# Kernel optimization log

Measured on AMD Instinct MI355X. Metric: run time of the kernel, lower is better.

Reference implementation:

```python
import math
import jax, jax.numpy as jnp
import numpy as np

CHUNK = 64  # chunk_size


def sinusoidal_pe(L, H):
    # PositionalEncoding2: standard sinusoidal table added to input (eval mode, no dropout)
    pos = jnp.arange(L, dtype=jnp.float32)[:, None]
    div = jnp.exp(jnp.arange(0, H, 2, dtype=jnp.float32) * (-math.log(10000.0) / H))
    pe = jnp.zeros((L, H), dtype=jnp.float32)
    pe = pe.at[:, 0::2].set(jnp.sin(pos * div))
    pe = pe.at[:, 1::2].set(jnp.cos(pos * div))
    return pe


def setup_inputs() -> dict:
    key = jax.random.key(0)
    ks = jax.random.split(key, 8)
    B, T, D, H, Dv = 8, 4096, 512, 512, 512
    s = 0.02
    return {
        "data": jax.random.normal(ks[0], (B, T, D), dtype=jnp.float32),
        "v0": jax.random.normal(ks[1], (B, Dv), dtype=jnp.float32),
        "v1": jax.random.normal(ks[2], (B, Dv), dtype=jnp.float32),
        "W_embed": jax.random.normal(ks[3], (D, H), dtype=jnp.float32) * s,
        "b_embed": jnp.zeros((H,), dtype=jnp.float32),
        "Wx": jax.random.normal(ks[4], (H, 2), dtype=jnp.float32) * s,
        "Wv": jax.random.normal(ks[5], (Dv, 2), dtype=jnp.float32) * s,
        "b_f": jnp.zeros((2,), dtype=jnp.float32),
    }


def reference(data, v0, v1, W_embed, b_embed, Wx, Wv, b_f):
    B, T, D = data.shape
    H = W_embed.shape[1]
    n_chunks = T // CHUNK  # chunks per batch row

    # add_pos: Linear embed + positional encoding, scaled by sqrt(chunk_size)
    h = data @ W_embed + b_embed                       # [B, T, H]
    h = (h + sinusoidal_pe(T, H)[None]) * math.sqrt(CHUNK)

    x = h.reshape(B * n_chunks, CHUNK, H)              # chunked view

    key = jax.random.key(42)
    F = None
    for i, v in enumerate((v0, v1)):
        v_rep = jnp.repeat(v, n_chunks, axis=0)        # [B*n_chunks, Dv]
        # filter model: per-token 2-way logits conditioned on chunk value vector
        logits = x @ Wx + (v_rep @ Wv)[:, None, :] + b_f  # [B*n_chunks, CHUNK, 2]
        # StochasticMultinomialTensor.sample(): gumbel-max one-hot, straight-through
        g = jax.random.gumbel(jax.random.fold_in(key, i), logits.shape, dtype=logits.dtype)
        hard = jax.nn.one_hot(jnp.argmax(logits + g, axis=-1), 2, dtype=logits.dtype)
        soft = jax.nn.softmax(logits, axis=-1)
        samp = soft + jax.lax.stop_gradient(hard - soft)
        f = samp[:, :, 0].reshape(B, T)                # de_chunk -> [B, T]
        F = f if F is None else F * f

    mask = F > 0.5                                     # [B, T]
    vals = h * F[..., None]                            # data[F>0.5] * F scaling

    # ragged compaction: stable-sort selected tokens to the front of each row
    order = jnp.argsort((~mask).astype(jnp.int32), axis=1)   # stable
    packed = jnp.take_along_axis(vals, order[:, :, None], axis=1)  # [B, T, H]
    lens = mask.sum(-1)                                # per-row selected count
    keep = jnp.arange(T)[None, :] < lens[:, None]
    # pad_sequence equivalent, padded to T (superset of max(lens)); zeros beyond lens
    return packed * keep[..., None]
```

## Files before the change

### kernel.cpp

```cpp
#include <hip/hip_runtime.h>
#include <stdint.h>


#define NB 8
#define NT 4096
#define ND 512
#define NH 512
#define NTOK (NB * NT)

typedef __attribute__((ext_vector_type(8))) short short8;
typedef __attribute__((ext_vector_type(4))) float f32x4;

#define WS_WEX   0
#define WS_PEX   8192
#define WS_VWV   73728
#define WS_LENS  76048
#define WS_WT    76096
#define WS_MASK  731456
#define WS_ABF16 1310720

__device__ inline void threefry2x32(uint32_t k0, uint32_t k1, uint32_t x0, uint32_t x1,
                                    uint32_t& y0, uint32_t& y1) {
  uint32_t ks2 = k0 ^ k1 ^ 0x1BD11BDAu;
  x0 += k0; x1 += k1;
#define TFR(r) { x0 += x1; x1 = (x1 << (r)) | (x1 >> (32 - (r))); x1 ^= x0; }
  TFR(13) TFR(15) TFR(26) TFR(6)   x0 += k1;  x1 += ks2 + 1u;
  TFR(17) TFR(29) TFR(16) TFR(24)  x0 += ks2; x1 += k0 + 2u;
  TFR(13) TFR(15) TFR(26) TFR(6)   x0 += k0;  x1 += k1 + 3u;
  TFR(17) TFR(29) TFR(16) TFR(24)  x0 += k1;  x1 += ks2 + 4u;
  TFR(13) TFR(15) TFR(26) TFR(6)   x0 += ks2; x1 += k0 + 5u;
#undef TFR
  y0 = x0; y1 = x1;
}

__device__ inline uint32_t rb_bits(uint32_t k0, uint32_t k1, uint32_t idx) {
  uint32_t y0, y1;
  threefry2x32(k0, k1, 0u, idx, y0, y1);
  return y0 ^ y1;
}

__device__ inline double gumbel_from_bits(uint32_t bits) {
  uint32_t m = bits >> 9;
  float u = m ? (float)m * 1.1920928955078125e-07f : 1.17549435082228751e-38f;
  double lu = log((double)u);
  return -log(-lu);
}

__device__ inline uint16_t f2bf(float f) {
  union { float f; uint32_t u; } v; v.f = f;
  uint32_t u = v.u;
  return (uint16_t)((u + 0x7FFFu + ((u >> 16) & 1u)) >> 16);
}

__device__ inline double wredd(double v) {
#pragma unroll
  for (int o = 32; o > 0; o >>= 1) v += __shfl_xor(v, o, 64);
  return v;
}

__device__ inline void fsincos(double x, double& sv, double& cv) {
  const double invpio2 = 6.36619772367581382433e-01;
  const double pio2_1  = 1.57079632673412561417e+00;
  const double pio2_1t = 6.07710050650619224932e-11;
  double fn = floor(x * invpio2 + 0.5);
  int n = (int)fn;
  double r = x - fn * pio2_1;
  r = r - fn * pio2_1t;
  double z = r * r;
  const double S1 = -1.66666666666666324348e-01, S2 = 8.33333333332248946124e-03,
               S3 = -1.98412698298579493134e-04, S4 = 2.75573137070700676789e-06,
               S5 = -2.50507602534068634195e-08, S6 = 1.58969099521155010221e-10;
  const double C1 = 4.16666666666666019037e-02, C2 = -1.38888888888741095749e-03,
               C3 = 2.48015872894767294178e-05, C4 = -2.75573143513906633035e-07,
               C5 = 2.08757232129817482790e-09, C6 = -1.13596475577881948265e-11;
  double ss = r + r * z * (S1 + z * (S2 + z * (S3 + z * (S4 + z * (S5 + z * S6)))));
  double cc = 1.0 + z * (-0.5 + z * (C1 + z * (C2 + z * (C3 + z * (C4 + z * (C5 + z * C6))))));
  int q = n & 3;
  sv = (q == 0) ? ss : (q == 1) ? cc : (q == 2) ? -ss : -cc;
  cv = (q == 0) ? cc : (q == 1) ? -ss : (q == 2) ? -cc : ss;
}

__device__ inline void gld_lds16(const void* g, void* l) {
  __builtin_amdgcn_global_load_lds(
      (const __attribute__((address_space(1))) void*)g,
      (__attribute__((address_space(3))) void*)l, 16, 0, 0);
}

__global__ __launch_bounds__(64) void k_prep(
    const float* __restrict__ v0, const float* __restrict__ v1,
    const float* __restrict__ W, const float* __restrict__ be,
    const float* __restrict__ Wx, const float* __restrict__ Wv,
    char* __restrict__ ws) {
  double* Wex = (double*)(ws + WS_WEX);
  double* pex = (double*)(ws + WS_PEX);
  double* vWv = (double*)(ws + WS_VWV);
  uint16_t* Wt = (uint16_t*)(ws + WS_WT);
  __shared__ double divs[256];
  int blk = blockIdx.x;
  int lane = threadIdx.x;

  if (blk < 512) {
    int d = blk;
    double a0 = 0.0, a1 = 0.0;
    for (int it = 0; it < 8; ++it) {
      int h = it * 64 + lane;
      double w = (double)W[d * 512 + h];
      a0 += w * (double)Wx[2 * h];
      a1 += w * (double)Wx[2 * h + 1];
    }
    a0 = wredd(a0); a1 = wredd(a1);
    if (lane == 0) { Wex[2 * d] = a0; Wex[2 * d + 1] = a1; }
  } else if (blk < 4608) {
    const double c2 = -2.0 * 9.210340371976184 / 512.0;
    for (int it = 0; it < 4; ++it) {
      int f = it * 64 + lane;
      divs[f] = exp((double)f * c2);
    }
    __syncthreads();
    int t = blk - 512;
    double td = (double)t;
    double a0 = 0.0, a1 = 0.0;
    for (int it = 0; it < 8; ++it) {
      int h = it * 64 + lane;
      double dv = divs[h >> 1];
      double sv, cv;
      fsincos(td * dv, sv, cv);
      double pe = (h & 1) ? cv : sv;
      double pb = pe + (double)be[h];
      a0 += pb * (double)Wx[2 * h];
      a1 += pb * (double)Wx[2 * h + 1];
    }
    a0 = wredd(a0); a1 = wredd(a1);
    if (lane == 0) { pex[2 * t] = a0; pex[2 * t + 1] = a1; }
  } else if (blk < 4624) {
    int q = blk - 4608;
    int i = q >> 3, b = q & 7;
    const float* v = i ? v1 : v0;
    double a0 = 0.0, a1 = 0.0;
    for (int it = 0; it < 8; ++it) {
      int d = it * 64 + lane;
      double x = (double)v[b * 512 + d];
      a0 += x * (double)Wv[2 * d];
      a1 += x * (double)Wv[2 * d + 1];
    }
    a0 = wredd(a0); a1 = wredd(a1);
    if (lane == 0) { vWv[(i * 8 + b) * 2] = a0; vWv[(i * 8 + b) * 2 + 1] = a1; }
  } else {
    int kk = blk - 4624;
    for (int it = 0; it < 8; ++it) {
      int n = it * 64 + lane;
      Wt[(size_t)n * 512 + kk] = f2bf(W[kk * 512 + n]);
    }
  }
}

__global__ __launch_bounds__(512) void k_dot(
    const float* __restrict__ data, const float* __restrict__ bfp,
    const char* __restrict__ wsc, int* __restrict__ mask,
    uint16_t* __restrict__ Abf) {
  const double* Wex = (const double*)(wsc + WS_WEX);
  const double* pex = (const double*)(wsc + WS_PEX);
  const double* vWv = (const double*)(wsc + WS_VWV);

  int wid = threadIdx.x >> 6;
  int lane = threadIdx.x & 63;
  int k0 = blockIdx.x * 8;
  int k = k0 + wid;

  const float4* dp = (const float4*)(data + (size_t)k * 512 + lane * 8);
  float4 f0 = dp[0], f1 = dp[1];
  float xv[8] = {f0.x, f0.y, f0.z, f0.w, f1.x, f1.y, f1.z, f1.w};

  const double* wx = Wex + lane * 16;
  double d0 = 0.0, d1 = 0.0;
#pragma unroll
  for (int u = 0; u < 8; ++u) {
    double x = (double)xv[u];
    d0 += x * wx[2 * u];
    d1 += x * wx[2 * u + 1];
  }
  d0 = wredd(d0); d1 = wredd(d1);

  __shared__ double dsh[8][2];
  __shared__ int keep_sh[8];
  if (lane == 0) { dsh[wid][0] = d0; dsh[wid][1] = d1; }
  __syncthreads();

  if (wid == 0) {
    int dec = 0;
    if (lane < 32) {
      int tt = lane >> 2, i = (lane >> 1) & 1, j = lane & 1;
      int kk = k0 + tt;
      int bb = kk >> 12, ttok = kk & 4095;
      uint32_t key0, key1;
      threefry2x32(0u, 42u, 0u, (uint32_t)i, key0, key1);
      double dj = dsh[tt][j];
      double lj = 8.0 * (dj + pex[ttok * 2 + j]) + (double)bfp[j];
      double z = lj + vWv[(i * 8 + bb) * 2 + j]
                   + gumbel_from_bits(rb_bits(key0, key1, (uint32_t)(2 * kk + j)));
      double zo = __shfl_xor(z, 1, 64);
      dec = (z >= zo) ? 1 : 0;
    }
    unsigned long long bal = __ballot(dec);
    if (lane < 8) {
      int keep = (int)((bal >> (lane * 4)) & (bal >> (lane * 4 + 2)) & 1ULL);
      keep_sh[lane] = keep;
      mask[k0 + lane] = keep;
    }
  }
  __syncthreads();

  if (keep_sh[wid]) {
    short8 o;
#pragma unroll
    for (int u = 0; u < 8; ++u) o[u] = (short)f2bf(xv[u]);
    *(short8*)(Abf + (size_t)k * 512 + lane * 8) = o;
  }
}

__global__ __launch_bounds__(1024) void k_scan(
    int* __restrict__ morder, int* __restrict__ lens) {
  __shared__ int wsum[16];
  int b = blockIdx.x, tid = threadIdx.x;
  int wid = tid >> 6, lane = tid & 63;
  int t0 = tid * 4;
  int4 mv = *(const int4*)(morder + b * 4096 + t0);
  int m[4] = {mv.x, mv.y, mv.z, mv.w};
  int p = m[0] + m[1] + m[2] + m[3];

  int s = p;
#pragma unroll
  for (int off = 1; off < 64; off <<= 1) {
    int v = __shfl_up(s, off, 64);
    if (lane >= off) s += v;
  }
  if (lane == 63) wsum[wid] = s;
  __syncthreads();
  if (wid == 0) {
    int w = (lane < 16) ? wsum[lane] : 0;
#pragma unroll
    for (int off = 1; off < 16; off <<= 1) {
      int v = __shfl_up(w, off, 64);
      if (lane >= off) w += v;
    }
    if (lane < 16) wsum[lane] = w;
  }
  __syncthreads();
  int run = ((wid > 0) ? wsum[wid - 1] : 0) + s - p;
  int base = b * 4096;
  if (m[0]) morder[base + run] = t0 + 0;
  run += m[0];
  if (m[1]) morder[base + run] = t0 + 1;
  run += m[1];
  if (m[2]) morder[base + run] = t0 + 2;
  run += m[2];
  if (m[3]) morder[base + run] = t0 + 3;
  if (tid == 1023) lens[b] = wsum[15];
}

__global__ __launch_bounds__(256) void k_zero(
    const char* __restrict__ wsc, float* __restrict__ out) {
  const int* lens = (const int*)(wsc + WS_LENS);
  int b = blockIdx.y;
  int j = blockIdx.x * 4 + (threadIdx.x >> 6);
  if (j < lens[b]) return;
  int lane = threadIdx.x & 63;
  float4 z = {0.f, 0.f, 0.f, 0.f};
  float* op = out + ((size_t)(b * 4096 + j)) * 512 + lane * 8;
  *(float4*)op = z;
  *(float4*)(op + 4) = z;
}

#define BM 128
#define BN 128
#define BK 32

__global__ __launch_bounds__(256) void k_gemm(
    const uint16_t* __restrict__ Abf, const float* __restrict__ be,
    const char* __restrict__ wsc, float* __restrict__ out) {
  const uint16_t* Wt = (const uint16_t*)(wsc + WS_WT);
  const int* order = (const int*)(wsc + WS_MASK);
  const int* lens = (const int*)(wsc + WS_LENS);

  int cum[9];
  cum[0] = 0;
#pragma unroll
  for (int i = 0; i < 8; ++i) cum[i + 1] = cum[i] + lens[i];
  int S = cum[8];

  int bid = blockIdx.x;
  int nb = bid & 3;
  int G = (bid >> 2) * BM;
  if (G >= S) return;

  int tid = threadIdx.x;
  int wave = tid >> 6, lane = tid & 63;
  int wm = wave & 1, wn = wave >> 1;
  int quad = lane >> 4, l15 = lane & 15;
  int srow = lane >> 2;
  int scol = (lane & 3) * 8;

  __shared__ __align__(16) uint16_t As[BM * BK];
  __shared__ __align__(16) uint16_t Bs[BN * BK];

  f32x4 acc[4][4] = {};

  int lr = wave * 16 + srow;
  int pg0 = G + lr, pg1 = pg0 + 64;
  int b0 = 0, pin0 = pg0, b1 = 0, pin1 = pg1;
#pragma unroll
  for (int i = 1; i < 8; ++i) {
    if (pg0 >= cum[i]) { b0 = i; pin0 = pg0 - cum[i]; }
    if (pg1 >= cum[i]) { b1 = i; pin1 = pg1 - cum[i]; }
  }
  if (pg0 >= S) { b0 = 0; pin0 = 0; }
  if (pg1 >= S) { b1 = 0; pin1 = 0; }
  int t0r = order[(b0 << 12) + pin0];
  int t1r = order[(b1 << 12) + pin1];
  const uint16_t* a0p = Abf + (((size_t)(b0 << 12) + t0r) << 9) + scol;
  const uint16_t* a1p = Abf + (((size_t)(b1 << 12) + t1r) << 9) + scol;
  const uint16_t* gB = Wt + (size_t)(nb * BN) * 512;
  const uint16_t* b0p = gB + (size_t)lr * 512 + scol;
  const uint16_t* b1p = b0p + (size_t)64 * 512;

  uint16_t* lA = As + (size_t)(wave * 16) * BK;
  uint16_t* lB = Bs + (size_t)(wave * 16) * BK;

  for (int k0 = 0; k0 < 512; k0 += BK) {
    gld_lds16(a0p + k0, lA);
    gld_lds16(a1p + k0, lA + 64 * BK);
    gld_lds16(b0p + k0, lB);
    gld_lds16(b1p + k0, lB + 64 * BK);
    __syncthreads();

    short8 af[4], bfr[4];
#pragma unroll
    for (int mi = 0; mi < 4; ++mi)
      af[mi] = *(const short8*)&As[(wm * 64 + mi * 16 + l15) * BK + quad * 8];
#pragma unroll
    for (int ni = 0; ni < 4; ++ni)
      bfr[ni] = *(const short8*)&Bs[(wn * 64 + ni * 16 + l15) * BK + quad * 8];
#pragma unroll
    for (int mi = 0; mi < 4; ++mi)
#pragma unroll
      for (int ni = 0; ni < 4; ++ni)
        acc[mi][ni] = __builtin_amdgcn_mfma_f32_16x16x32_bf16(af[mi], bfr[ni], acc[mi][ni], 0, 0, 0);
    __syncthreads();
  }

  int* ords = (int*)As;
  int* orows = (int*)Bs;
  if (tid < 128) {
    int pg = G + tid;
    int bb = 0, pp = pg;
#pragma unroll
    for (int i = 1; i < 8; ++i)
      if (pg >= cum[i]) { bb = i; pp = pg - cum[i]; }
    bool val = pg < S;
    ords[tid] = val ? order[(bb << 12) + pp] : 0;
    orows[tid] = val ? ((bb << 12) + pp) : -1;
  }
  __syncthreads();

  const float c1 = -0.01798894603951557739f;
#pragma unroll
  for (int ni = 0; ni < 4; ++ni) {
    int n = nb * BN + wn * 64 + ni * 16 + l15;
    float dv = __expf((float)(n & ~1) * c1);
    float ben = be[n];
#pragma unroll
    for (int mi = 0; mi < 4; ++mi) {
#pragma unroll
      for (int r = 0; r < 4; ++r) {
        int lrow = wm * 64 + mi * 16 + quad * 4 + r;
        int oj = orows[lrow];
        if (oj >= 0) {
          int t = ords[lrow];
          float ph = (float)t * dv;
          float pe = (n & 1) ? __cosf(ph) : __sinf(ph);
          out[((size_t)oj) * 512 + n] = 8.0f * (acc[mi][ni][r] + ben + pe);
        }
      }
    }
  }
}

extern "C" void kernel_launch(void* const* d_in, const int* in_sizes, int n_in,
                              void* d_out, int out_size, void* d_ws, size_t ws_size,
                              hipStream_t stream) {
  const float* data = (const float*)d_in[0];
  const float* v0   = (const float*)d_in[1];
  const float* v1   = (const float*)d_in[2];
  const float* W    = (const float*)d_in[3];
  const float* be   = (const float*)d_in[4];
  const float* Wx   = (const float*)d_in[5];
  const float* Wv   = (const float*)d_in[6];
  const float* bfp  = (const float*)d_in[7];
  char* ws = (char*)d_ws;
  float* out = (float*)d_out;
  uint16_t* Abf = (uint16_t*)(ws + WS_ABF16);

  hipLaunchKernelGGL(k_prep, dim3(5136), dim3(64), 0, stream, v0, v1, W, be, Wx, Wv, ws);
  hipLaunchKernelGGL(k_dot, dim3(4096), dim3(512), 0, stream,
                     data, bfp, (const char*)ws, (int*)(ws + WS_MASK), Abf);
  hipLaunchKernelGGL(k_scan, dim3(8), dim3(1024), 0, stream,
                     (int*)(ws + WS_MASK), (int*)(ws + WS_LENS));
  hipLaunchKernelGGL(k_zero, dim3(1024, 8), dim3(256), 0, stream, (const char*)ws, out);
  hipLaunchKernelGGL(k_gemm, dim3(1024), dim3(256), 0, stream,
                     Abf, be, (const char*)ws, out);
}
```

Baseline: 188.2 us.

## Restructure k_dot to process four tokens per wave without block barriers

Each wave now handles four tokens on its own, keeping the Wx weights in registers across them and making the Gumbel keep decision inside the wave, so the shared-memory exchange and both __syncthreads are gone. The kernel launches 2048 blocks of 256 threads instead of 4096 blocks of 512. It also writes the bf16 copy of every token unconditionally instead of only kept tokens, which adds write traffic. Loads change from float4 vectors to strided scalar accesses, which may reduce memory efficiency.

Measured after the change: 171.6 us. 1.1x faster.

```diff
diff --git a/kernel.cpp b/kernel.cpp
--- a/kernel.cpp
+++ b/kernel.cpp
@@ -154,7 +154,7 @@
   }
 }
 
-__global__ __launch_bounds__(512) void k_dot(
+__global__ __launch_bounds__(256) void k_dot(
     const float* __restrict__ data, const float* __restrict__ bfp,
     const char* __restrict__ wsc, int* __restrict__ mask,
     uint16_t* __restrict__ Abf) {
@@ -164,58 +164,61 @@
 
   int wid = threadIdx.x >> 6;
   int lane = threadIdx.x & 63;
-  int k0 = blockIdx.x * 8;
-  int k = k0 + wid;
-
-  const float4* dp = (const float4*)(data + (size_t)k * 512 + lane * 8);
-  float4 f0 = dp[0], f1 = dp[1];
-  float xv[8] = {f0.x, f0.y, f0.z, f0.w, f1.x, f1.y, f1.z, f1.w};
-
-  const double* wx = Wex + lane * 16;
-  double d0 = 0.0, d1 = 0.0;
+  int kbase = (blockIdx.x * 4 + wid) * 4;
+
+  double w0[8], w1[8];
 #pragma unroll
   for (int u = 0; u < 8; ++u) {
-    double x = (double)xv[u];
-    d0 += x * wx[2 * u];
-    d1 += x * wx[2 * u + 1];
-  }
-  d0 = wredd(d0); d1 = wredd(d1);
-
-  __shared__ double dsh[8][2];
-  __shared__ int keep_sh[8];
-  if (lane == 0) { dsh[wid][0] = d0; dsh[wid][1] = d1; }
-  __syncthreads();
-
-  if (wid == 0) {
-    int dec = 0;
-    if (lane < 32) {
-      int tt = lane >> 2, i = (lane >> 1) & 1, j = lane & 1;
-      int kk = k0 + tt;
-      int bb = kk >> 12, ttok = kk & 4095;
-      uint32_t key0, key1;
-      threefry2x32(0u, 42u, 0u, (uint32_t)i, key0, key1);
-      double dj = dsh[tt][j];
-      double lj = 8.0 * (dj + pex[ttok * 2 + j]) + (double)bfp[j];
-      double z = lj + vWv[(i * 8 + bb) * 2 + j]
-                   + gumbel_from_bits(rb_bits(key0, key1, (uint32_t)(2 * kk + j)));
-      double zo = __shfl_xor(z, 1, 64);
-      dec = (z >= zo) ? 1 : 0;
-    }
-    unsigned long long bal = __ballot(dec);
-    if (lane < 8) {
-      int keep = (int)((bal >> (lane * 4)) & (bal >> (lane * 4 + 2)) & 1ULL);
-      keep_sh[lane] = keep;
-      mask[k0 + lane] = keep;
-    }
-  }
-  __syncthreads();
-
-  if (keep_sh[wid]) {
-    short8 o;
-#pragma unroll
-    for (int u = 0; u < 8; ++u) o[u] = (short)f2bf(xv[u]);
-    *(short8*)(Abf + (size_t)k * 512 + lane * 8) = o;
-  }
+    double2 wv = *(const double2*)(Wex + 2 * (u * 64 + lane));
+    w0[u] = wv.x; w1[u] = wv.y;
+  }
+
+  double d0s[4], d1s[4];
+#pragma unroll
+  for (int tt = 0; tt < 4; ++tt) {
+    int k = kbase + tt;
+    const float* dpt = data + (size_t)k * 512 + lane;
+    float x[8];
+#pragma unroll
+    for (int u = 0; u < 8; ++u) x[u] = dpt[u * 64];
+
+    uint16_t* ap = Abf + (size_t)k * 512 + lane;
+#pragma unroll
+    for (int u = 0; u < 8; ++u) ap[u * 64] = f2bf(x[u]);
+
+    double d0 = 0.0, d1 = 0.0;
+#pragma unroll
+    for (int u = 0; u < 8; ++u) {
+      double xd = (double)x[u];
+      d0 += xd * w0[u];
+      d1 += xd * w1[u];
+    }
+    d0s[tt] = wredd(d0);
+    d1s[tt] = wredd(d1);
+  }
+
+  int dec = 0;
+  if (lane < 16) {
+    int tt = lane >> 2, i = (lane >> 1) & 1, j = lane & 1;
+    double da = (tt & 2) ? ((tt & 1) ? d0s[3] : d0s[2])
+                         : ((tt & 1) ? d0s[1] : d0s[0]);
+    double db = (tt & 2) ? ((tt & 1) ? d1s[3] : d1s[2])
+                         : ((tt & 1) ? d1s[1] : d1s[0]);
+    double dj = j ? db : da;
+    int kk = kbase + tt;
+    int bb = kk >> 12, ttok = kk & 4095;
+    uint32_t key0, key1;
+    threefry2x32(0u, 42u, 0u, (uint32_t)i, key0, key1);
+    double lj = 8.0 * (dj + pex[ttok * 2 + j]) + (double)bfp[j];
+    double z = lj + vWv[(i * 8 + bb) * 2 + j]
+                 + gumbel_from_bits(rb_bits(key0, key1, (uint32_t)(2 * kk + j)));
+    double zo = __shfl_xor(z, 1, 64);
+    dec = (z >= zo) ? 1 : 0;
+  }
+  unsigned long long bal = __ballot(dec);
+  if (lane < 4)
+    mask[kbase + lane] =
+        (int)((bal >> (lane * 4)) & (bal >> (lane * 4 + 2)) & 1ULL);
 }
 
 __global__ __launch_bounds__(1024) void k_scan(
@@ -401,7 +404,7 @@
   uint16_t* Abf = (uint16_t*)(ws + WS_ABF16);
 
   hipLaunchKernelGGL(k_prep, dim3(5136), dim3(64), 0, stream, v0, v1, W, be, Wx, Wv, ws);
-  hipLaunchKernelGGL(k_dot, dim3(4096), dim3(512), 0, stream,
+  hipLaunchKernelGGL(k_dot, dim3(2048), dim3(256), 0, stream,
                      data, bfp, (const char*)ws, (int*)(ws + WS_MASK), Abf);
   hipLaunchKernelGGL(k_scan, dim3(8), dim3(1024), 0, stream,
                      (int*)(ws + WS_MASK), (int*)(ws + WS_LENS));
```
